# Performance work log

Hardware: AMD Instinct MI355X
Metric: run time of the kernel (lower is better)

## Reference

```python
import jax, jax.numpy as jnp
import numpy as np

T, B, E = 2048, 16, 1024   # time, batch, embed_dim (fairseq T x B x C layout)
CDIM = 1024                # conv_dim
H = 16                     # num_heads
K = 31                     # kernel_size, padding_l = K-1 (causal left pad)


def _xavier(k, shape):
    fan_out, fan_in = shape
    lim = float(np.sqrt(6.0 / (fan_in + fan_out)))
    return jax.random.uniform(k, shape, jnp.float32, -lim, lim)


def setup_inputs() -> dict:
    key = jax.random.key(0)
    ks = jax.random.split(key, 5)
    return {
        "x": jax.random.normal(ks[0], (T, B, E), jnp.float32),
        "w1": _xavier(ks[1], (CDIM, E)),
        "b1": jnp.zeros((CDIM,), jnp.float32),
        "ww": _xavier(ks[2], (H * K, CDIM)),  # DynamicConv weight_linear
        "bw": jnp.zeros((H * K,), jnp.float32),
        "w2": _xavier(ks[3], (E, CDIM)),
        "b2": jnp.zeros((E,), jnp.float32),
        "gamma": jnp.ones((E,), jnp.float32),
        "beta": jnp.zeros((E,), jnp.float32),
    }


def layer_norm(x, g, b, eps=1e-5):
    m = x.mean(-1, keepdims=True)
    v = ((x - m) ** 2).mean(-1, keepdims=True)
    return (x - m) * jax.lax.rsqrt(v + eps) * g + b


def dynamic_conv(h, ww, bw):
    # h: [T, B, C]; per-position softmax kernel weights shared across R=C/H channels per head
    Tn, Bn, C = h.shape
    R = C // H
    w = jax.nn.softmax((h @ ww.T + bw).reshape(Tn, Bn, H, K), axis=-1)  # [T,B,H,K]
    hp = jnp.pad(h.reshape(Tn, Bn, H, R), ((K - 1, 0), (0, 0), (0, 0), (0, 0)))
    # out[t] = sum_k w[t,:,:,k] * h[t + k - (K-1)]  (causal banded aggregation)
    acc = jnp.zeros((Tn, Bn, H, R), h.dtype)
    for k in range(K):  # fixed small kernel-size loop, not a data-dim loop
        acc = acc + w[:, :, :, k:k + 1] * hp[k:k + Tn]
    return acc.reshape(Tn, Bn, C)


def reference(x, w1, b1, ww, bw, w2, b2, gamma, beta):
    # eval mode: all dropouts are identity; normalize_before=False -> LN after residual
    h = x @ w1.T + b1            # linear1: [T,B,E] -> [T,B,CDIM]
    h = dynamic_conv(h, ww, bw)  # DynamicConv, weight_softmax=True, no conv bias
    h = h @ w2.T + b2            # linear2: back to embed_dim
    return layer_norm(x + h, gamma, beta)
```

## Files before the change

### kernel.cpp

```cpp
#include <hip/hip_runtime.h>

#define T_DIM 2048
#define B_DIM 16
#define E_DIM 1024
#define CD    1024
#define NH    16
#define KSZ   31
#define M_DIM 32768
#define SLICE 131072
#define BSTRIDE 2097152

typedef unsigned int u32;
typedef unsigned short u16;
typedef __attribute__((ext_vector_type(8))) __bf16 bf16x8;
typedef __attribute__((ext_vector_type(4))) float f32x4;
typedef __attribute__((ext_vector_type(4))) float fvec4;
typedef __attribute__((ext_vector_type(8))) unsigned short us8;
typedef __attribute__((ext_vector_type(4))) unsigned short us4;
typedef __attribute__((ext_vector_type(4))) unsigned int ui4;

__device__ __forceinline__ float bf2f(u16 u) {
  union { float f; u32 i; } c; c.i = ((u32)u) << 16; return c.f;
}
__device__ __forceinline__ u16 f2bf(float f) {
  union { float f; u32 i; } c; c.f = f;
  u32 u = c.i;
  u += 0x7fffu + ((u >> 16) & 1u);
  return (u16)(u >> 16);
}

#define GLDS(gp, lp)                                                        \
  __builtin_amdgcn_global_load_lds(                                         \
      (__attribute__((address_space(1))) void*)(gp),                        \
      (__attribute__((address_space(3))) void*)(lp), 16, 0, 0)

__global__ __launch_bounds__(256) void zfill(u16* __restrict__ z) {
  ((ui4*)z)[threadIdx.x] = (ui4)(0u);
}

__global__ __launch_bounds__(256) void cvt_f32_bf16(const float* __restrict__ src,
                                                    u16* __restrict__ dst, int n4) {
  int i = blockIdx.x * 256 + threadIdx.x;
  int stride = gridDim.x * 256;
  const fvec4* s4 = (const fvec4*)src;
  us4* d4 = (us4*)dst;
  for (; i < n4; i += stride) {
    fvec4 v = s4[i];
    us4 o;
    o[0] = f2bf(v[0]); o[1] = f2bf(v[1]); o[2] = f2bf(v[2]); o[3] = f2bf(v[3]);
    d4[i] = o;
  }
}

__global__ __launch_bounds__(256) void cvt_x_tr(const float* __restrict__ x,
                                                u16* __restrict__ xbt) {
  int rr = blockIdx.x;
  int t = rr >> 4, b = rr & 15;
  const fvec4* src = (const fvec4*)(x + (size_t)rr * E_DIM);
  us4* dst = (us4*)(xbt + ((size_t)b * T_DIM + t) * E_DIM);
  fvec4 v = src[threadIdx.x];
  us4 o;
  o[0] = f2bf(v[0]); o[1] = f2bf(v[1]); o[2] = f2bf(v[2]); o[3] = f2bf(v[3]);
  dst[threadIdx.x] = o;
}

template<int OUT_MODE, int GUARD_N, int A_CONV>
__global__ __launch_bounds__(512, 2) void gemm256(
    const u16* __restrict__ A, const u16* __restrict__ B,
    const float* __restrict__ bias, void* __restrict__ Cout,
    int N, int K, int ldc, int ntn)
{
  __shared__ u16 sA[2][256 * 64];
  __shared__ u16 sB[2][256 * 64];
  const int tid = threadIdx.x;
  const int lane = tid & 63;
  const int wid = tid >> 6;
  const int wr = wid >> 2;
  const int wc = wid & 3;

  const int swz = (blockIdx.x & 7) * (gridDim.x >> 3) + (blockIdx.x >> 3);
  const int bm = (swz / ntn) * 256;
  const int bn = (swz % ntn) * 256;

  const int srow = tid >> 3;
  const int scol = (tid & 7) * 8;
  const int scols = scol ^ ((srow & 7) << 3);

  const u16* gA[4];
  #pragma unroll
  for (int st = 0; st < 4; st++) {
    int rr = bm + st * 64 + srow;
    if (A_CONV)
      gA[st] = A + (size_t)(rr >> 11) * BSTRIDE + (size_t)(rr & 2047) * 64 + scols;
    else
      gA[st] = A + (size_t)rr * K + scols;
  }
  const u16* gB[4];
  #pragma unroll
  for (int st = 0; st < 4; st++) {
    int br = bn + st * 64 + srow;
    if (GUARD_N) br = min(br, N - 1);
    gB[st] = B + (size_t)br * K + scols;
  }
  const int sdst = (tid >> 3) * 64 + scol;

  f32x4 acc[8][4];
  #pragma unroll
  for (int i = 0; i < 8; i++)
    #pragma unroll
    for (int j = 0; j < 4; j++) acc[i][j] = (f32x4)(0.0f);

  const int fr = lane & 15;
  const int g8 = (lane >> 4) * 8;
  const int sx = (fr & 7) << 3;

  const int NT = K >> 6;
  int buf = 0;

  #pragma unroll
  for (int st = 0; st < 4; st++) GLDS(gB[st], &sB[0][st * 4096 + sdst]);
  GLDS(gA[0], &sA[0][0 * 4096 + sdst]);
  GLDS(gA[2], &sA[0][2 * 4096 + sdst]);
  GLDS(gA[1], &sA[0][1 * 4096 + sdst]);
  GLDS(gA[3], &sA[0][3 * 4096 + sdst]);
  asm volatile("s_waitcnt vmcnt(0)" ::: "memory");
  __builtin_amdgcn_s_barrier();

  for (int kt = 0; kt < NT; kt++) {
    const bool more = (kt + 1 < NT);
    const size_t koA = A_CONV ? (size_t)(kt + 1) * SLICE : (size_t)(kt + 1) * 64;
    const size_t koB = (size_t)(kt + 1) * 64;
    u16* dA = &sA[buf ^ 1][0];
    u16* dB = &sB[buf ^ 1][0];

    bf16x8 bF[4][2];
    #pragma unroll
    for (int n = 0; n < 4; n++)
      #pragma unroll
      for (int kh = 0; kh < 2; kh++) {
        int row = wc * 64 + n * 16 + fr;
        bF[n][kh] = *(const bf16x8*)&sB[buf][row * 64 + ((kh * 32 + g8) ^ sx)];
      }
    bf16x8 aF[2][2];
    #pragma unroll
    for (int mi = 0; mi < 2; mi++)
      #pragma unroll
      for (int kh = 0; kh < 2; kh++) {
        int row = wr * 128 + mi * 16 + fr;
        aF[mi][kh] = *(const bf16x8*)&sA[buf][row * 64 + ((kh * 32 + g8) ^ sx)];
      }
    if (more) {
      GLDS(gB[0] + koB, dB + 0 * 4096 + sdst);
      GLDS(gB[1] + koB, dB + 1 * 4096 + sdst);
      GLDS(gB[2] + koB, dB + 2 * 4096 + sdst);
      GLDS(gB[3] + koB, dB + 3 * 4096 + sdst);
      GLDS(gA[0] + koA, dA + 0 * 4096 + sdst);
      GLDS(gA[2] + koA, dA + 2 * 4096 + sdst);
    }
    __builtin_amdgcn_s_barrier();
    asm volatile("s_waitcnt lgkmcnt(0)" ::: "memory");
    __builtin_amdgcn_sched_barrier(0);
    __builtin_amdgcn_s_setprio(1);
    #pragma unroll
    for (int mi = 0; mi < 2; mi++)
      #pragma unroll
      for (int n = 0; n < 4; n++)
        #pragma unroll
        for (int kh = 0; kh < 2; kh++)
          acc[mi][n] = __builtin_amdgcn_mfma_f32_16x16x32_bf16(aF[mi][kh], bF[n][kh], acc[mi][n], 0, 0, 0);
    __builtin_amdgcn_s_setprio(0);
    __builtin_amdgcn_sched_barrier(0);
    __builtin_amdgcn_s_barrier();

    #pragma unroll
    for (int p = 1; p < 4; p++) {
      bf16x8 aG[2][2];
      #pragma unroll
      for (int mi = 0; mi < 2; mi++)
        #pragma unroll
        for (int kh = 0; kh < 2; kh++) {
          int row = wr * 128 + (2 * p + mi) * 16 + fr;
          aG[mi][kh] = *(const bf16x8*)&sA[buf][row * 64 + ((kh * 32 + g8) ^ sx)];
        }
      if (p == 1 && more) {
        GLDS(gA[1] + koA, dA + 1 * 4096 + sdst);
        GLDS(gA[3] + koA, dA + 3 * 4096 + sdst);
      }
      __builtin_amdgcn_s_barrier();
      asm volatile("s_waitcnt lgkmcnt(0)" ::: "memory");
      __builtin_amdgcn_sched_barrier(0);
      __builtin_amdgcn_s_setprio(1);
      #pragma unroll
      for (int mi = 0; mi < 2; mi++)
        #pragma unroll
        for (int n = 0; n < 4; n++)
          #pragma unroll
          for (int kh = 0; kh < 2; kh++)
            acc[2 * p + mi][n] = __builtin_amdgcn_mfma_f32_16x16x32_bf16(aG[mi][kh], bF[n][kh], acc[2 * p + mi][n], 0, 0, 0);
      __builtin_amdgcn_s_setprio(0);
      __builtin_amdgcn_sched_barrier(0);
      if (p == 1) {
        if (more) { asm volatile("s_waitcnt vmcnt(8)" ::: "memory"); }
        else      { asm volatile("s_waitcnt vmcnt(0)" ::: "memory"); }
      }
      if (p == 3 && more) {
        asm volatile("s_waitcnt vmcnt(2)" ::: "memory");
      }
      __builtin_amdgcn_s_barrier();
    }
    buf ^= 1;
  }

  const int orow0 = bm + wr * 128 + (lane >> 4) * 4;
  const int ocol0 = bn + wc * 64 + fr;
  #pragma unroll
  for (int m = 0; m < 8; m++) {
    #pragma unroll
    for (int n = 0; n < 4; n++) {
      #pragma unroll
      for (int q = 0; q < 4; q++) {
        int row = orow0 + m * 16 + q;
        int col = ocol0 + n * 16;
        if (!GUARD_N || col < N) {
          float v = acc[m][n][q] + bias[col];
          if (OUT_MODE == 1) {
            ((u16*)Cout)[(size_t)row * ldc + col] = f2bf(v);
          } else if (OUT_MODE == 2) {
            int bb = row >> 11, t = row & 2047;
            int hh = col / 31, kk = col - hh * 31;
            ((float*)Cout)[((size_t)((bb * NH + hh) * T_DIM + t)) * 32 + kk] = v;
          } else {
            int bb = row >> 11, t = row & 2047;
            ((u16*)Cout)[(size_t)((bb << 4) + (col >> 6)) * SLICE + (size_t)t * 64 + (col & 63)] = f2bf(v);
          }
        }
      }
    }
  }
}

__global__ __launch_bounds__(256) void dconv(const u16* __restrict__ h1,
                                             const float* __restrict__ wt,
                                             const u16* __restrict__ zreg,
                                             u16* __restrict__ outc)
{
  constexpr int TT = 64, HALO = 30, SW = 33;
  int bid = blockIdx.x;
  int tt = bid & 31;
  int s  = bid >> 5;
  int t0 = tt * TT;
  __shared__ u16 hl[96 * 64];
  __shared__ float wl[TT * SW];
  int tid = threadIdx.x;

  const u16* slice = h1 + (size_t)s * SLICE;
  #pragma unroll
  for (int it = 0; it < 3; it++) {
    int c = it * 256 + tid;
    int row = t0 - HALO + (c >> 3);
    const u16* src = slice + (size_t)row * 64 + (c & 7) * 8;
    if (row < 0) src = zreg + (c & 7) * 8;
    GLDS(src, hl + c * 8);
  }
  const float* wsrc = wt + ((size_t)s * T_DIM + t0) * 32;
  #pragma unroll
  for (int it = 0; it < 2; it++) {
    int j = it * 1024 + tid * 4;
    f32x4 v = *(const f32x4*)(wsrc + j);
    int row = j >> 5, col = j & 31;
    *(f32x4*)(&wl[row * SW + col]) = v;
  }
  __syncthreads();

  if (tid < TT) {
    float* p = wl + tid * SW;
    float v[KSZ];
    float mx = -1e30f;
    #pragma unroll
    for (int k = 0; k < KSZ; k++) { v[k] = p[k]; mx = fmaxf(mx, v[k]); }
    float sum = 0.f;
    #pragma unroll
    for (int k = 0; k < KSZ; k++) { v[k] = __expf(v[k] - mx); sum += v[k]; }
    float inv = 1.0f / sum;
    #pragma unroll
    for (int k = 0; k < KSZ; k++) p[k] = v[k] * inv;
  }
  __syncthreads();

  int rb = (tid & 7) * 8;
  int tl = tid >> 3;

  #pragma unroll
  for (int half = 0; half < 2; half++) {
    const int tb = tl + half * 32;
    const float* wp = wl + tb * SW;
    const u16* hb = hl + tb * 64 + rb;
    float acc[8];
    #pragma unroll
    for (int e = 0; e < 8; e++) acc[e] = 0.f;
    #pragma unroll
    for (int k = 0; k < KSZ; k++) {
      us8 hv = *(const us8*)(hb + k * 64);
      float w = wp[k];
      #pragma unroll
      for (int e = 0; e < 8; e++) acc[e] += w * bf2f(hv[e]);
    }
    us8 o;
    #pragma unroll
    for (int e = 0; e < 8; e++) o[e] = f2bf(acc[e]);
    *(us8*)(outc + (size_t)s * SLICE + (size_t)(t0 + tb) * 64 + rb) = o;
  }
}

__global__ __launch_bounds__(256) void ln_res(const float* __restrict__ x,
                                              const u16* __restrict__ hb,
                                              float* __restrict__ out,
                                              const float* __restrict__ gamma,
                                              const float* __restrict__ beta)
{
  int mp = blockIdx.x;
  int b = mp >> 11, t = mp & 2047;
  int xrow = t * 16 + b;
  const fvec4* xr = (const fvec4*)(x + (size_t)xrow * E_DIM);
  const us4* hr = (const us4*)(hb + (size_t)mp * E_DIM);
  fvec4* yr = (fvec4*)(out + (size_t)xrow * E_DIM);
  int tid = threadIdx.x;
  us4 hv = hr[tid];
  fvec4 xv = xr[tid];
  fvec4 s;
  #pragma unroll
  for (int e = 0; e < 4; e++) s[e] = xv[e] + bf2f(hv[e]);
  float sum = s[0] + s[1] + s[2] + s[3];
  float sq  = s[0]*s[0] + s[1]*s[1] + s[2]*s[2] + s[3]*s[3];
  #pragma unroll
  for (int off = 32; off >= 1; off >>= 1) {
    sum += __shfl_xor(sum, off, 64);
    sq  += __shfl_xor(sq, off, 64);
  }
  __shared__ float red[8];
  int lane = tid & 63, wid = tid >> 6;
  if (lane == 0) { red[wid] = sum; red[4 + wid] = sq; }
  __syncthreads();
  sum = red[0] + red[1] + red[2] + red[3];
  sq  = red[4] + red[5] + red[6] + red[7];
  float mean = sum * (1.0f / E_DIM);
  float var  = sq * (1.0f / E_DIM) - mean * mean;
  float rstd = rsqrtf(var + 1e-5f);
  fvec4 g = ((const fvec4*)gamma)[tid];
  fvec4 be = ((const fvec4*)beta)[tid];
  fvec4 o;
  #pragma unroll
  for (int e = 0; e < 4; e++) o[e] = (s[e] - mean) * rstd * g[e] + be[e];
  yr[tid] = o;
}

extern "C" void kernel_launch(void* const* d_in, const int* in_sizes, int n_in,
                              void* d_out, int out_size, void* d_ws, size_t ws_size,
                              hipStream_t stream)
{
  const float* x     = (const float*)d_in[0];
  const float* w1    = (const float*)d_in[1];
  const float* b1    = (const float*)d_in[2];
  const float* ww    = (const float*)d_in[3];
  const float* bw    = (const float*)d_in[4];
  const float* w2    = (const float*)d_in[5];
  const float* b2    = (const float*)d_in[6];
  const float* gamma = (const float*)d_in[7];
  const float* beta  = (const float*)d_in[8];
  float* out = (float*)d_out;

  char* ws = (char*)d_ws;
  u16*   xbt  = (u16*)(ws);
  u16*   h1p  = (u16*)(ws + ((size_t)64 << 20));
  float* wt   = (float*)(ws + ((size_t)128 << 20));
  u16*   w1b  = (u16*)(ws + ((size_t)192 << 20));
  u16*   w2b  = (u16*)(ws + ((size_t)194 << 20));
  u16*   wwb  = (u16*)(ws + ((size_t)196 << 20));
  u16*   zreg = (u16*)(ws + ((size_t)198 << 20));
  u16*   convp = xbt;
  u16*   h2p  = h1p;

  zfill<<<1, 256, 0, stream>>>(zreg);
  cvt_x_tr<<<32768, 256, 0, stream>>>(x, xbt);
  cvt_f32_bf16<<<1024, 256, 0, stream>>>(w1, w1b, (CD * E_DIM) / 4);
  cvt_f32_bf16<<<1024, 256, 0, stream>>>(w2, w2b, (E_DIM * CD) / 4);
  cvt_f32_bf16<<<512,  256, 0, stream>>>(ww, wwb, (NH * KSZ * CD) / 4);

  gemm256<3, 0, 0><<<512, 512, 0, stream>>>(xbt, w1b, b1, h1p, CD, E_DIM, 0, 4);
  gemm256<2, 1, 1><<<256, 512, 0, stream>>>(h1p, wwb, bw, wt, NH * KSZ, CD, 0, 2);
  dconv<<<8192, 256, 0, stream>>>(h1p, wt, zreg, convp);
  gemm256<1, 0, 1><<<512, 512, 0, stream>>>(convp, w2b, b2, h2p, E_DIM, CD, E_DIM, 4);
  ln_res<<<32768, 256, 0, stream>>>(x, h2p, out, gamma, beta);
}
```

Before: 384.1 us.

## Fuse x fp32-to-bf16 transpose into first GEMM and store conv logits as bf16

Removes the separate cvt_x_tr pass. The first GEMM now reads fp32 x directly in its T×B layout, converts it to bf16 in registers and writes it into swizzled LDS, with the prefetch schedule rearranged to interleave these register loads with the B-tile async loads. The weight-linear GEMM also writes its softmax logits as bf16 instead of fp32, halving the traffic that dconv reads back. This trades a full write and read of the bf16 copy of x for extra VGPR pressure and synchronous global loads in the GEMM main loop, and slightly lowers the precision of the logits.

After: 373.1 us. 1.03x faster.

```diff
diff --git a/kernel.cpp b/kernel.cpp
--- a/kernel.cpp
+++ b/kernel.cpp
@@ -52,21 +52,9 @@
   }
 }
 
-__global__ __launch_bounds__(256) void cvt_x_tr(const float* __restrict__ x,
-                                                u16* __restrict__ xbt) {
-  int rr = blockIdx.x;
-  int t = rr >> 4, b = rr & 15;
-  const fvec4* src = (const fvec4*)(x + (size_t)rr * E_DIM);
-  us4* dst = (us4*)(xbt + ((size_t)b * T_DIM + t) * E_DIM);
-  fvec4 v = src[threadIdx.x];
-  us4 o;
-  o[0] = f2bf(v[0]); o[1] = f2bf(v[1]); o[2] = f2bf(v[2]); o[3] = f2bf(v[3]);
-  dst[threadIdx.x] = o;
-}
-
-template<int OUT_MODE, int GUARD_N, int A_CONV>
+template<int OUT_MODE, int GUARD_N, int A_MODE>
 __global__ __launch_bounds__(512, 2) void gemm256(
-    const u16* __restrict__ A, const u16* __restrict__ B,
+    const void* __restrict__ Av, const u16* __restrict__ B,
     const float* __restrict__ bias, void* __restrict__ Cout,
     int N, int K, int ldc, int ntn)
 {
@@ -85,15 +73,25 @@
   const int srow = tid >> 3;
   const int scol = (tid & 7) * 8;
   const int scols = scol ^ ((srow & 7) << 3);
+  const int sdst   = srow * 64 + scol;
+  const int sdst_s = srow * 64 + scols;
+
+  const u16* Ab = (const u16*)Av;
+  const float* Af = (const float*)Av;
 
   const u16* gA[4];
+  const float* gX[4];
   #pragma unroll
   for (int st = 0; st < 4; st++) {
     int rr = bm + st * 64 + srow;
-    if (A_CONV)
-      gA[st] = A + (size_t)(rr >> 11) * BSTRIDE + (size_t)(rr & 2047) * 64 + scols;
-    else
-      gA[st] = A + (size_t)rr * K + scols;
+    if (A_MODE == 1) {
+      gA[st] = Ab + (size_t)(rr >> 11) * BSTRIDE + (size_t)(rr & 2047) * 64 + scols;
+      gX[st] = nullptr;
+    } else {
+      int t = rr & 2047, b = rr >> 11;
+      gX[st] = Af + (size_t)(t * 16 + b) * 1024 + scol;
+      gA[st] = nullptr;
+    }
   }
   const u16* gB[4];
   #pragma unroll
@@ -102,7 +100,6 @@
     if (GUARD_N) br = min(br, N - 1);
     gB[st] = B + (size_t)br * K + scols;
   }
-  const int sdst = (tid >> 3) * 64 + scol;
 
   f32x4 acc[8][4];
   #pragma unroll
@@ -119,19 +116,37 @@
 
   #pragma unroll
   for (int st = 0; st < 4; st++) GLDS(gB[st], &sB[0][st * 4096 + sdst]);
-  GLDS(gA[0], &sA[0][0 * 4096 + sdst]);
-  GLDS(gA[2], &sA[0][2 * 4096 + sdst]);
-  GLDS(gA[1], &sA[0][1 * 4096 + sdst]);
-  GLDS(gA[3], &sA[0][3 * 4096 + sdst]);
-  asm volatile("s_waitcnt vmcnt(0)" ::: "memory");
+  if (A_MODE == 1) {
+    #pragma unroll
+    for (int st = 0; st < 4; st++) GLDS(gA[st], &sA[0][st * 4096 + sdst]);
+    asm volatile("s_waitcnt vmcnt(0)" ::: "memory");
+  } else {
+    fvec4 q[4][2];
+    #pragma unroll
+    for (int st = 0; st < 4; st++) {
+      q[st][0] = *(const fvec4*)(gX[st]);
+      q[st][1] = *(const fvec4*)(gX[st] + 4);
+    }
+    #pragma unroll
+    for (int st = 0; st < 4; st++) {
+      us8 o;
+      #pragma unroll
+      for (int e = 0; e < 4; e++) { o[e] = f2bf(q[st][0][e]); o[e + 4] = f2bf(q[st][1][e]); }
+      *(us8*)&sA[0][st * 4096 + sdst_s] = o;
+    }
+    asm volatile("s_waitcnt vmcnt(0)" ::: "memory");
+    asm volatile("s_waitcnt lgkmcnt(0)" ::: "memory");
+  }
   __builtin_amdgcn_s_barrier();
 
   for (int kt = 0; kt < NT; kt++) {
     const bool more = (kt + 1 < NT);
-    const size_t koA = A_CONV ? (size_t)(kt + 1) * SLICE : (size_t)(kt + 1) * 64;
     const size_t koB = (size_t)(kt + 1) * 64;
+    const size_t koA = (size_t)(kt + 1) * SLICE;
+    const size_t koX = (size_t)(kt + 1) * 64;
     u16* dA = &sA[buf ^ 1][0];
     u16* dB = &sB[buf ^ 1][0];
+    fvec4 xa[4][2];
 
     bf16x8 bF[4][2];
     #pragma unroll
@@ -152,10 +167,10 @@
     if (more) {
       GLDS(gB[0] + koB, dB + 0 * 4096 + sdst);
       GLDS(gB[1] + koB, dB + 1 * 4096 + sdst);
-      GLDS(gB[2] + koB, dB + 2 * 4096 + sdst);
-      GLDS(gB[3] + koB, dB + 3 * 4096 + sdst);
-      GLDS(gA[0] + koA, dA + 0 * 4096 + sdst);
-      GLDS(gA[2] + koA, dA + 2 * 4096 + sdst);
+      if (A_MODE == 2) {
+        xa[0][0] = *(const fvec4*)(gX[0] + koX); xa[0][1] = *(const fvec4*)(gX[0] + koX + 4);
+        xa[1][0] = *(const fvec4*)(gX[1] + koX); xa[1][1] = *(const fvec4*)(gX[1] + koX + 4);
+      }
     }
     __builtin_amdgcn_s_barrier();
     asm volatile("s_waitcnt lgkmcnt(0)" ::: "memory");
@@ -172,19 +187,22 @@
     __builtin_amdgcn_sched_barrier(0);
     __builtin_amdgcn_s_barrier();
 
-    #pragma unroll
-    for (int p = 1; p < 4; p++) {
+    {
       bf16x8 aG[2][2];
       #pragma unroll
       for (int mi = 0; mi < 2; mi++)
         #pragma unroll
         for (int kh = 0; kh < 2; kh++) {
-          int row = wr * 128 + (2 * p + mi) * 16 + fr;
+          int row = wr * 128 + (2 + mi) * 16 + fr;
           aG[mi][kh] = *(const bf16x8*)&sA[buf][row * 64 + ((kh * 32 + g8) ^ sx)];
         }
-      if (p == 1 && more) {
-        GLDS(gA[1] + koA, dA + 1 * 4096 + sdst);
-        GLDS(gA[3] + koA, dA + 3 * 4096 + sdst);
+      if (more) {
+        GLDS(gB[2] + koB, dB + 2 * 4096 + sdst);
+        GLDS(gB[3] + koB, dB + 3 * 4096 + sdst);
+        if (A_MODE == 2) {
+          xa[2][0] = *(const fvec4*)(gX[2] + koX); xa[2][1] = *(const fvec4*)(gX[2] + koX + 4);
+          xa[3][0] = *(const fvec4*)(gX[3] + koX); xa[3][1] = *(const fvec4*)(gX[3] + koX + 4);
+        }
       }
       __builtin_amdgcn_s_barrier();
       asm volatile("s_waitcnt lgkmcnt(0)" ::: "memory");
@@ -196,14 +214,96 @@
         for (int n = 0; n < 4; n++)
           #pragma unroll
           for (int kh = 0; kh < 2; kh++)
-            acc[2 * p + mi][n] = __builtin_amdgcn_mfma_f32_16x16x32_bf16(aG[mi][kh], bF[n][kh], acc[2 * p + mi][n], 0, 0, 0);
+            acc[2 + mi][n] = __builtin_amdgcn_mfma_f32_16x16x32_bf16(aG[mi][kh], bF[n][kh], acc[2 + mi][n], 0, 0, 0);
       __builtin_amdgcn_s_setprio(0);
       __builtin_amdgcn_sched_barrier(0);
-      if (p == 1) {
-        if (more) { asm volatile("s_waitcnt vmcnt(8)" ::: "memory"); }
+      if (A_MODE == 1) {
+        if (more) { asm volatile("s_waitcnt vmcnt(4)" ::: "memory"); }
         else      { asm volatile("s_waitcnt vmcnt(0)" ::: "memory"); }
       }
-      if (p == 3 && more) {
+      __builtin_amdgcn_s_barrier();
+    }
+
+    {
+      bf16x8 aG[2][2];
+      #pragma unroll
+      for (int mi = 0; mi < 2; mi++)
+        #pragma unroll
+        for (int kh = 0; kh < 2; kh++) {
+          int row = wr * 128 + (4 + mi) * 16 + fr;
+          aG[mi][kh] = *(const bf16x8*)&sA[buf][row * 64 + ((kh * 32 + g8) ^ sx)];
+        }
+      if (more) {
+        if (A_MODE == 1) {
+          GLDS(gA[0] + koA, dA + 0 * 4096 + sdst);
+          GLDS(gA[2] + koA, dA + 2 * 4096 + sdst);
+        } else {
+          #pragma unroll
+          for (int st = 0; st < 2; st++) {
+            us8 o;
+            #pragma unroll
+            for (int e = 0; e < 4; e++) { o[e] = f2bf(xa[st][0][e]); o[e + 4] = f2bf(xa[st][1][e]); }
+            *(us8*)(dA + st * 4096 + sdst_s) = o;
+          }
+        }
+      }
+      __builtin_amdgcn_s_barrier();
+      asm volatile("s_waitcnt lgkmcnt(0)" ::: "memory");
+      __builtin_amdgcn_sched_barrier(0);
+      __builtin_amdgcn_s_setprio(1);
+      #pragma unroll
+      for (int mi = 0; mi < 2; mi++)
+        #pragma unroll
+        for (int n = 0; n < 4; n++)
+          #pragma unroll
+          for (int kh = 0; kh < 2; kh++)
+            acc[4 + mi][n] = __builtin_amdgcn_mfma_f32_16x16x32_bf16(aG[mi][kh], bF[n][kh], acc[4 + mi][n], 0, 0, 0);
+      __builtin_amdgcn_s_setprio(0);
+      __builtin_amdgcn_sched_barrier(0);
+      __builtin_amdgcn_s_barrier();
+    }
+
+    {
+      bf16x8 aG[2][2];
+      #pragma unroll
+      for (int mi = 0; mi < 2; mi++)
+        #pragma unroll
+        for (int kh = 0; kh < 2; kh++) {
+          int row = wr * 128 + (6 + mi) * 16 + fr;
+          aG[mi][kh] = *(const bf16x8*)&sA[buf][row * 64 + ((kh * 32 + g8) ^ sx)];
+        }
+      if (more) {
+        if (A_MODE == 1) {
+          GLDS(gA[1] + koA, dA + 1 * 4096 + sdst);
+          GLDS(gA[3] + koA, dA + 3 * 4096 + sdst);
+        } else {
+          #pragma unroll
+          for (int st = 2; st < 4; st++) {
+            us8 o;
+            #pragma unroll
+            for (int e = 0; e < 4; e++) { o[e] = f2bf(xa[st][0][e]); o[e + 4] = f2bf(xa[st][1][e]); }
+            *(us8*)(dA + st * 4096 + sdst_s) = o;
+          }
+        }
+      }
+      if (A_MODE == 2) {
+        if (more) { asm volatile("s_waitcnt vmcnt(0)" ::: "memory"); }
+        asm volatile("s_waitcnt lgkmcnt(0)" ::: "memory");
+      }
+      __builtin_amdgcn_s_barrier();
+      asm volatile("s_waitcnt lgkmcnt(0)" ::: "memory");
+      __builtin_amdgcn_sched_barrier(0);
+      __builtin_amdgcn_s_setprio(1);
+      #pragma unroll
+      for (int mi = 0; mi < 2; mi++)
+        #pragma unroll
+        for (int n = 0; n < 4; n++)
+          #pragma unroll
+          for (int kh = 0; kh < 2; kh++)
+            acc[6 + mi][n] = __builtin_amdgcn_mfma_f32_16x16x32_bf16(aG[mi][kh], bF[n][kh], acc[6 + mi][n], 0, 0, 0);
+      __builtin_amdgcn_s_setprio(0);
+      __builtin_amdgcn_sched_barrier(0);
+      if (A_MODE == 1 && more) {
         asm volatile("s_waitcnt vmcnt(2)" ::: "memory");
       }
       __builtin_amdgcn_s_barrier();
@@ -228,7 +328,7 @@
           } else if (OUT_MODE == 2) {
             int bb = row >> 11, t = row & 2047;
             int hh = col / 31, kk = col - hh * 31;
-            ((float*)Cout)[((size_t)((bb * NH + hh) * T_DIM + t)) * 32 + kk] = v;
+            ((u16*)Cout)[((size_t)((bb * NH + hh) * T_DIM + t)) * 32 + kk] = f2bf(v);
           } else {
             int bb = row >> 11, t = row & 2047;
             ((u16*)Cout)[(size_t)((bb << 4) + (col >> 6)) * SLICE + (size_t)t * 64 + (col & 63)] = f2bf(v);
@@ -240,7 +340,7 @@
 }
 
 __global__ __launch_bounds__(256) void dconv(const u16* __restrict__ h1,
-                                             const float* __restrict__ wt,
+                                             const u16* __restrict__ wt,
                                              const u16* __restrict__ zreg,
                                              u16* __restrict__ outc)
 {
@@ -262,13 +362,13 @@
     if (row < 0) src = zreg + (c & 7) * 8;
     GLDS(src, hl + c * 8);
   }
-  const float* wsrc = wt + ((size_t)s * T_DIM + t0) * 32;
-  #pragma unroll
-  for (int it = 0; it < 2; it++) {
-    int j = it * 1024 + tid * 4;
-    f32x4 v = *(const f32x4*)(wsrc + j);
+  {
+    const u16* wsrc = wt + ((size_t)s * T_DIM + t0) * 32;
+    int j = tid * 8;
+    us8 v = *(const us8*)(wsrc + j);
     int row = j >> 5, col = j & 31;
-    *(f32x4*)(&wl[row * SW + col]) = v;
+    #pragma unroll
+    for (int e = 0; e < 8; e++) wl[row * SW + col + e] = bf2f(v[e]);
   }
   __syncthreads();
 
@@ -370,23 +470,21 @@
   float* out = (float*)d_out;
 
   char* ws = (char*)d_ws;
-  u16*   xbt  = (u16*)(ws);
+  u16*   convp = (u16*)(ws);
   u16*   h1p  = (u16*)(ws + ((size_t)64 << 20));
-  float* wt   = (float*)(ws + ((size_t)128 << 20));
+  u16*   wt   = (u16*)(ws + ((size_t)128 << 20));
   u16*   w1b  = (u16*)(ws + ((size_t)192 << 20));
   u16*   w2b  = (u16*)(ws + ((size_t)194 << 20));
   u16*   wwb  = (u16*)(ws + ((size_t)196 << 20));
   u16*   zreg = (u16*)(ws + ((size_t)198 << 20));
-  u16*   convp = xbt;
   u16*   h2p  = h1p;
 
   zfill<<<1, 256, 0, stream>>>(zreg);
-  cvt_x_tr<<<32768, 256, 0, stream>>>(x, xbt);
   cvt_f32_bf16<<<1024, 256, 0, stream>>>(w1, w1b, (CD * E_DIM) / 4);
   cvt_f32_bf16<<<1024, 256, 0, stream>>>(w2, w2b, (E_DIM * CD) / 4);
   cvt_f32_bf16<<<512,  256, 0, stream>>>(ww, wwb, (NH * KSZ * CD) / 4);
 
-  gemm256<3, 0, 0><<<512, 512, 0, stream>>>(xbt, w1b, b1, h1p, CD, E_DIM, 0, 4);
+  gemm256<3, 0, 2><<<512, 512, 0, stream>>>(x, w1b, b1, h1p, CD, E_DIM, 0, 4);
   gemm256<2, 1, 1><<<256, 512, 0, stream>>>(h1p, wwb, bw, wt, NH * KSZ, CD, 0, 2);
   dconv<<<8192, 256, 0, stream>>>(h1p, wt, zreg, convp);
   gemm256<1, 0, 1><<<512, 512, 0, stream>>>(convp, w2b, b2, h2p, E_DIM, CD, E_DIM, 4);
```
